# Performance work log

Measured on AMD Instinct MI355X. Metric: run time of the kernel, lower is better.

## Reference

```python
import jax, jax.numpy as jnp
from jax import lax
import numpy as np

DIVISOR = 2.0  # init kwarg 'divisor'


def setup_inputs() -> dict:
    key = jax.random.key(0)
    k1, k2, k3, k4 = jax.random.split(key, 4)
    x = jax.random.normal(k1, (8, 32, 32, 64, 64), dtype=jnp.float32)        # N,C_in,D,H,W
    conv_weight = jax.random.normal(k2, (64, 32, 3, 3, 3), dtype=jnp.float32)  # O,I,kD,kH,kW
    conv_bias = jax.random.normal(k3, (64,), dtype=jnp.float32)
    bias = jax.random.normal(k4, (64, 1, 1, 1), dtype=jnp.float32)           # post bias (per out-channel)
    return {"x": x, "conv_weight": conv_weight, "conv_bias": conv_bias, "bias": bias}


def reference(x, conv_weight, conv_bias, bias):
    # Valid 3D conv, stride 1 (matches the CUDA kernel's sliding window)
    y = lax.conv_general_dilated(
        x, conv_weight,
        window_strides=(1, 1, 1), padding='VALID',
        dimension_numbers=('NCDHW', 'OIDHW', 'NCDHW'))
    # (conv + conv_bias) / divisor + post_bias, then sum over out-channels
    y = (y + conv_bias[None, :, None, None, None]) * (1.0 / DIVISOR) \
        + bias.reshape(1, -1, 1, 1, 1)
    return jnp.sum(y, axis=1)  # (N, D_out, H_out, W_out)
```

## Files before the change

kernel.cpp:

```cpp
#include <hip/hip_runtime.h>


#define XD 32
#define XH 64
#define XW 64
#define DOUT 30
#define HOUT 62
#define WOUT 62
#define CH_STRIDE (XD * XH * XW)
#define WBUF_FLOATS 2048

__device__ __forceinline__ float nextlane(float v) {
  return __int_as_float(
      __builtin_amdgcn_mov_dpp(__float_as_int(v), 0x101, 0xF, 0xF, true));
}

__global__ __launch_bounds__(256, 2)
void conv3d_chansum_kernel(const float* __restrict__ x,
                           const float* __restrict__ cw,
                           const float* __restrict__ cb,
                           const float* __restrict__ pb,
                           float* __restrict__ out) {
  __shared__ float wavebuf[4][2][WBUF_FLOATS];
  __shared__ float wl[897];

  const int tid  = threadIdx.x;
  const int wid  = tid >> 6;
  const int lane = tid & 63;
  const int hb = blockIdx.x, db = blockIdx.y, n = blockIdx.z;
  const int h0 = hb * 8, d0 = db * 4;
  const int s  = tid & 7;
  const int ht = (tid >> 3) & 7;
  const bool alive = (d0 + wid) < DOUT;

  const float* xn = x + (size_t)n * (32u * CH_STRIDE);

  int soff[8];
#pragma unroll
  for (int i = 0; i < 8; ++i) {
    int k   = 64 * i + lane;
    int sd  = k / 160;
    int rem = k - sd * 160;
    int rr  = rem >> 4;
    int p   = rem & 15;
    int t1  = (11 * p) & 15;
    int csrc = (t1 < 8) ? (2 * t1) : (2 * ((11 * (p - 8)) & 15) + 1);
    int dd = min(d0 + wid + sd, XD - 1);
    int hh = min(h0 + rr, XH - 1);
    soff[i] = dd * (XH * XW) + hh * XW + csrc * 4;
  }

  auto stage = [&](float* buf, int ch) {
    const float* xnc = xn + (size_t)ch * CH_STRIDE;
#pragma unroll
    for (int i = 0; i < 8; ++i) {
      __builtin_amdgcn_global_load_lds(
          (const __attribute__((address_space(1))) void*)(xnc + soff[i]),
          (__attribute__((address_space(3))) void*)(buf + i * 256),
          16, 0, 0);
    }
  };

  if (alive) stage(&wavebuf[wid][0][0], 0);
  for (int e = tid; e < 864; e += 256) {
    int i = e / 27;
    int j = e - i * 27;
    float ssum = 0.f;
#pragma unroll 8
    for (int o = 0; o < 64; ++o) ssum += cw[o * 864 + e];
    wl[i * 28 + j] = 0.5f * ssum;
  }
  if (tid == 0) {
    float ssum = 0.f;
    for (int o = 0; o < 64; ++o) ssum += 0.5f * cb[o] + pb[o];
    wl[896] = ssum;
  }
  __syncthreads();
  if (!alive) return;

  const int P0 = (3 * s) & 15;
  const int P1 = (3 * s + 8) & 15;

  float acc[8];
#pragma unroll
  for (int j = 0; j < 8; ++j) acc[j] = 0.f;

#pragma unroll 1
  for (int ch = 0; ch < 32; ++ch) {
    const int chn = (ch < 31) ? ch + 1 : 31;
    stage(&wavebuf[wid][(ch + 1) & 1][0], chn);
    asm volatile("s_waitcnt vmcnt(8)" ::: "memory");
    __builtin_amdgcn_sched_barrier(0);

    const float* buf = &wavebuf[wid][ch & 1][0];
    float wr[28];
#pragma unroll
    for (int q = 0; q < 7; ++q)
      *(float4*)&wr[4 * q] = *(const float4*)&wl[ch * 28 + 4 * q];

#pragma unroll
    for (int kd = 0; kd < 3; ++kd) {
#pragma unroll
      for (int kh = 0; kh < 3; ++kh) {
        const int base = (kd * 10 + ht + kh) * 64;
        float4 a = *(const float4*)&buf[base + (P0 << 2)];
        float4 b = *(const float4*)&buf[base + (P1 << 2)];
        float x8 = nextlane(a.x);
        float x9 = nextlane(a.y);
        float xv[10] = {a.x, a.y, a.z, a.w, b.x, b.y, b.z, b.w, x8, x9};
        const int wb = kd * 9 + kh * 3;
#pragma unroll
        for (int j = 0; j < 8; ++j)
          acc[j] = fmaf(xv[j], wr[wb],
                   fmaf(xv[j + 1], wr[wb + 1],
                   fmaf(xv[j + 2], wr[wb + 2], acc[j])));
      }
    }

    asm volatile("s_waitcnt lgkmcnt(0)" ::: "memory");
    __builtin_amdgcn_sched_barrier(0);
  }

  const float Cc  = wl[896];
  const int   dow = d0 + wid, how = h0 + ht;
  if (how < HOUT) {
    float* op = out + (((size_t)n * DOUT + dow) * HOUT + how) * WOUT + s * 8;
    const int nw = min(8, WOUT - s * 8);
#pragma unroll
    for (int j = 0; j < 4; ++j) {
      if (2 * j < nw) {
        float2 v;
        v.x = acc[2 * j] + Cc;
        v.y = acc[2 * j + 1] + Cc;
        *(float2*)&op[2 * j] = v;
      }
    }
  }
}

extern "C" void kernel_launch(void* const* d_in, const int* in_sizes, int n_in,
                              void* d_out, int out_size, void* d_ws, size_t ws_size,
                              hipStream_t stream) {
  const float* x  = (const float*)d_in[0];
  const float* cw = (const float*)d_in[1];
  const float* cb = (const float*)d_in[2];
  const float* pb = (const float*)d_in[3];
  float* out = (float*)d_out;

  dim3 grid(8, 8, 8);
  conv3d_chansum_kernel<<<grid, 256, 0, stream>>>(x, cw, cb, pb, out);
}
```

Baseline: 224.6 us.

## Replace LDS-staged double buffer with direct register loads and smaller per-wave tiles

Drops the global_load_lds double-buffered staging and has each thread load its nine float4 input rows straight into registers every channel. Each thread now computes 4 outputs instead of 8, each wave covers a 4-row h slab, and the 1D grid uses a swizzled block order. Launch bounds rise to 4 blocks per CU because LDS use shrinks to the small weight table. This removes LDS traffic and waitcnt barriers, but loses the explicit prefetch overlap and reloads overlapping input rows from cache.

```diff
diff --git a/kernel.cpp b/kernel.cpp
--- a/kernel.cpp
+++ b/kernel.cpp
@@ -8,132 +8,118 @@
 #define HOUT 62
 #define WOUT 62
 #define CH_STRIDE (XD * XH * XW)
-#define WBUF_FLOATS 2048
 
 __device__ __forceinline__ float nextlane(float v) {
   return __int_as_float(
       __builtin_amdgcn_mov_dpp(__float_as_int(v), 0x101, 0xF, 0xF, true));
 }
 
-__global__ __launch_bounds__(256, 2)
-void conv3d_chansum_kernel(const float* __restrict__ x,
-                           const float* __restrict__ cw,
-                           const float* __restrict__ cb,
-                           const float* __restrict__ pb,
-                           float* __restrict__ out) {
-  __shared__ float wavebuf[4][2][WBUF_FLOATS];
-  __shared__ float wl[897];
+__global__ __launch_bounds__(256, 4)
+void conv3d_chansum_reg(const float* __restrict__ x,
+                        const float* __restrict__ cw,
+                        const float* __restrict__ cb,
+                        const float* __restrict__ pb,
+                        float* __restrict__ out) {
+  __shared__ float wl[1537];
 
   const int tid  = threadIdx.x;
   const int wid  = tid >> 6;
   const int lane = tid & 63;
-  const int hb = blockIdx.x, db = blockIdx.y, n = blockIdx.z;
-  const int h0 = hb * 8, d0 = db * 4;
-  const int s  = tid & 7;
-  const int ht = (tid >> 3) & 7;
-  const bool alive = (d0 + wid) < DOUT;
 
-  const float* xn = x + (size_t)n * (32u * CH_STRIDE);
+  const int bid = blockIdx.x;
+  const int swz = (bid & 7) * 128 + (bid >> 3);
 
-  int soff[8];
+  const int wslab = swz * 4 + wid;
+  const int n  = wslab >> 9;
+  const int d  = (wslab >> 4) & 31;
+  const int h0 = (wslab & 15) * 4;
+
+  const int s  = lane & 15;
+  const int ht = lane >> 4;
+  const bool alive = d < DOUT;
+
+  if (tid < 216) {
+    const float4* cw4 = (const float4*)(cw + 4 * tid);
+    float4 sum = {0.f, 0.f, 0.f, 0.f};
+#pragma unroll 8
+    for (int o = 0; o < 64; ++o) {
+      float4 v = cw4[o * 216];
+      sum.x += v.x; sum.y += v.y; sum.z += v.z; sum.w += v.w;
+    }
+    float vs[4] = {sum.x, sum.y, sum.z, sum.w};
 #pragma unroll
-  for (int i = 0; i < 8; ++i) {
-    int k   = 64 * i + lane;
-    int sd  = k / 160;
-    int rem = k - sd * 160;
-    int rr  = rem >> 4;
-    int p   = rem & 15;
-    int t1  = (11 * p) & 15;
-    int csrc = (t1 < 8) ? (2 * t1) : (2 * ((11 * (p - 8)) & 15) + 1);
-    int dd = min(d0 + wid + sd, XD - 1);
-    int hh = min(h0 + rr, XH - 1);
-    soff[i] = dd * (XH * XW) + hh * XW + csrc * 4;
+    for (int q = 0; q < 4; ++q) {
+      int e  = 4 * tid + q;
+      int i  = e / 27;
+      int r  = e - i * 27;
+      int kd = r / 9;
+      int t  = r - kd * 9;
+      wl[i * 48 + kd * 16 + t] = 0.5f * vs[q];
+    }
   }
-
-  auto stage = [&](float* buf, int ch) {
-    const float* xnc = xn + (size_t)ch * CH_STRIDE;
+  if (tid < 64) {
+    float v = 0.5f * cb[tid] + pb[tid];
 #pragma unroll
-    for (int i = 0; i < 8; ++i) {
-      __builtin_amdgcn_global_load_lds(
-          (const __attribute__((address_space(1))) void*)(xnc + soff[i]),
-          (__attribute__((address_space(3))) void*)(buf + i * 256),
-          16, 0, 0);
-    }
-  };
-
-  if (alive) stage(&wavebuf[wid][0][0], 0);
-  for (int e = tid; e < 864; e += 256) {
-    int i = e / 27;
-    int j = e - i * 27;
-    float ssum = 0.f;
-#pragma unroll 8
-    for (int o = 0; o < 64; ++o) ssum += cw[o * 864 + e];
-    wl[i * 28 + j] = 0.5f * ssum;
-  }
-  if (tid == 0) {
-    float ssum = 0.f;
-    for (int o = 0; o < 64; ++o) ssum += 0.5f * cb[o] + pb[o];
-    wl[896] = ssum;
+    for (int off = 32; off > 0; off >>= 1) v += __shfl_xor(v, off, 64);
+    if (tid == 0) wl[1536] = v;
   }
   __syncthreads();
   if (!alive) return;
 
-  const int P0 = (3 * s) & 15;
-  const int P1 = (3 * s + 8) & 15;
+  const float* xn = x + (size_t)n * (32u * CH_STRIDE);
 
-  float acc[8];
+  int soff[9];
 #pragma unroll
-  for (int j = 0; j < 8; ++j) acc[j] = 0.f;
+  for (int kd = 0; kd < 3; ++kd)
+#pragma unroll
+    for (int kh = 0; kh < 3; ++kh) {
+      int rc = min(h0 + ht + kh, XH - 1);
+      soff[kd * 3 + kh] = (d + kd) * (XH * XW) + rc * XW + 4 * s;
+    }
+
+  float acc[4] = {0.f, 0.f, 0.f, 0.f};
 
 #pragma unroll 1
   for (int ch = 0; ch < 32; ++ch) {
-    const int chn = (ch < 31) ? ch + 1 : 31;
-    stage(&wavebuf[wid][(ch + 1) & 1][0], chn);
-    asm volatile("s_waitcnt vmcnt(8)" ::: "memory");
-    __builtin_amdgcn_sched_barrier(0);
+    const float* xnc = xn + (size_t)ch * CH_STRIDE;
 
-    const float* buf = &wavebuf[wid][ch & 1][0];
-    float wr[28];
+    float4 a[9];
 #pragma unroll
-    for (int q = 0; q < 7; ++q)
-      *(float4*)&wr[4 * q] = *(const float4*)&wl[ch * 28 + 4 * q];
+    for (int i = 0; i < 9; ++i)
+      a[i] = *(const float4*)(xnc + soff[i]);
 
+    const float* wrow = &wl[ch * 48];
 #pragma unroll
     for (int kd = 0; kd < 3; ++kd) {
+      float4 w0 = *(const float4*)(wrow + kd * 16);
+      float4 w1 = *(const float4*)(wrow + kd * 16 + 4);
+      float  w8 = wrow[kd * 16 + 8];
+      float wt[9] = {w0.x, w0.y, w0.z, w0.w, w1.x, w1.y, w1.z, w1.w, w8};
 #pragma unroll
       for (int kh = 0; kh < 3; ++kh) {
-        const int base = (kd * 10 + ht + kh) * 64;
-        float4 a = *(const float4*)&buf[base + (P0 << 2)];
-        float4 b = *(const float4*)&buf[base + (P1 << 2)];
-        float x8 = nextlane(a.x);
-        float x9 = nextlane(a.y);
-        float xv[10] = {a.x, a.y, a.z, a.w, b.x, b.y, b.z, b.w, x8, x9};
-        const int wb = kd * 9 + kh * 3;
+        float4 av = a[kd * 3 + kh];
+        float x4v = nextlane(av.x);
+        float x5v = nextlane(av.y);
+        float xv[6] = {av.x, av.y, av.z, av.w, x4v, x5v};
 #pragma unroll
-        for (int j = 0; j < 8; ++j)
-          acc[j] = fmaf(xv[j], wr[wb],
-                   fmaf(xv[j + 1], wr[wb + 1],
-                   fmaf(xv[j + 2], wr[wb + 2], acc[j])));
+        for (int j = 0; j < 4; ++j)
+          acc[j] = fmaf(xv[j],     wt[kh * 3 + 0],
+                   fmaf(xv[j + 1], wt[kh * 3 + 1],
+                   fmaf(xv[j + 2], wt[kh * 3 + 2], acc[j])));
       }
     }
-
-    asm volatile("s_waitcnt lgkmcnt(0)" ::: "memory");
-    __builtin_amdgcn_sched_barrier(0);
   }
 
-  const float Cc  = wl[896];
-  const int   dow = d0 + wid, how = h0 + ht;
-  if (how < HOUT) {
-    float* op = out + (((size_t)n * DOUT + dow) * HOUT + how) * WOUT + s * 8;
-    const int nw = min(8, WOUT - s * 8);
-#pragma unroll
-    for (int j = 0; j < 4; ++j) {
-      if (2 * j < nw) {
-        float2 v;
-        v.x = acc[2 * j] + Cc;
-        v.y = acc[2 * j + 1] + Cc;
-        *(float2*)&op[2 * j] = v;
-      }
+  const float Cc = wl[1536];
+  const int h = h0 + ht;
+  if (h < HOUT) {
+    float* op = out + (((size_t)n * DOUT + d) * HOUT + h) * WOUT + 4 * s;
+    const int nw = min(4, WOUT - 4 * s);
+    float2 v0 = {acc[0] + Cc, acc[1] + Cc};
+    *(float2*)op = v0;
+    if (nw == 4) {
+      float2 v1 = {acc[2] + Cc, acc[3] + Cc};
+      *(float2*)(op + 2) = v1;
     }
   }
 }
@@ -147,6 +133,5 @@
   const float* pb = (const float*)d_in[3];
   float* out = (float*)d_out;
 
-  dim3 grid(8, 8, 8);
-  conv3d_chansum_kernel<<<grid, 256, 0, stream>>>(x, cw, cb, pb, out);
+  conv3d_chansum_reg<<<dim3(1024), 256, 0, stream>>>(x, cw, cb, pb, out);
 }
```

New measurement: 244.9 us. 9.0% more time.
